# Kernel tuning notes

Measured on AMD Instinct MI355X. Metric: run time of the kernel, lower is better.

Reference implementation:

```python
import jax, jax.numpy as jnp
import numpy as np
import math

B = 8
N_SURF_PER, N_LIG_PER = 5000, 128
N_SURF, N_LIG = B * N_SURF_PER, B * N_LIG_PER
N = N_SURF + N_LIG
HID, TDIM, NLAYERS = 512, 64, 6
E_MAX = 131072
RADIUS = 3.5
BOX = 24.1  # box edge so that radius-3.5 cross-degree ~64


def sinusoidal_emb(t, dim):
    # standard SinusoidalPosEmb: cat(sin, cos) over log-spaced freqs
    half = dim // 2
    freqs = jnp.exp(-math.log(10000.0) / (half - 1) * jnp.arange(half, dtype=t.dtype))
    ang = t[:, None] * freqs[None, :]
    return jnp.concatenate([jnp.sin(ang), jnp.cos(ang)], axis=-1)


def setup_inputs() -> dict:
    rng = np.random.default_rng(0)
    surf = rng.uniform(0.0, BOX, (B, N_SURF_PER, 3)).astype(np.float32)
    lig = rng.uniform(0.0, BOX, (B, N_LIG_PER, 3)).astype(np.float32)
    # radius_graph per batch; only surface->ligand edges survive filter_edges,
    # so we materialize exactly the cross edges (others are filtered to weight 0 anyway)
    srcs, dsts = [], []
    for b in range(B):
        d2 = ((surf[b][:, None, :] - lig[b][None, :, :]) ** 2).sum(-1)
        sj, li = np.nonzero(d2 <= RADIUS ** 2)
        srcs.append(b * N_SURF_PER + sj)
        dsts.append(N_SURF + b * N_LIG_PER + li)
    src = np.concatenate(srcs)
    dst = np.concatenate(dsts)
    E = min(len(src), E_MAX)
    edge_index = np.zeros((2, E_MAX), dtype=np.int32)  # pad with (0,0): filtered out
    edge_index[0, :E] = src[:E]
    edge_index[1, :E] = dst[:E]
    batch_surface = np.repeat(np.arange(B), N_SURF_PER).astype(np.int32)
    batch_ligand = np.repeat(np.arange(B), N_LIG_PER).astype(np.int32)

    ks = jax.random.split(jax.random.key(0), 10)

    def gl(k, shp, fan_in):
        return jax.random.normal(k, shp, jnp.float32) / np.sqrt(fan_in)

    return dict(
        surface_pos=jnp.asarray(surf.reshape(-1, 3)),
        init_ligand_pos=jnp.asarray(lig.reshape(-1, 3)),
        time=jax.random.uniform(ks[9], (N_LIG, 1), jnp.float32) * 1000.0,
        edge_index=jnp.asarray(edge_index),
        batch_surface=jnp.asarray(batch_surface),
        batch_ligand=jnp.asarray(batch_ligand),
        W_surf=gl(ks[0], (3, HID), 3), b_surf=jnp.zeros((HID,), jnp.float32),
        W_t1=gl(ks[1], (TDIM, 4 * TDIM), TDIM), b_t1=jnp.zeros((4 * TDIM,), jnp.float32),
        W_t2=gl(ks[2], (4 * TDIM, TDIM), 4 * TDIM), b_t2=jnp.zeros((TDIM,), jnp.float32),
        W_lig=gl(ks[3], (3, HID), 3), b_lig=jnp.zeros((HID,), jnp.float32),
        W_gate=gl(ks[4], (TDIM, HID), TDIM), b_gate=jnp.zeros((HID,), jnp.float32),
        W_hbias=gl(ks[5], (TDIM, HID), TDIM),
        W_gcn=gl(ks[6], (NLAYERS, HID, HID), HID), b_gcn=jnp.zeros((NLAYERS, HID), jnp.float32),
        W_pos=gl(ks[7], (HID, 3), HID), b_pos=jnp.zeros((3,), jnp.float32),
    )


def reference(surface_pos, init_ligand_pos, time, edge_index, batch_surface, batch_ligand,
              W_surf, b_surf, W_t1, b_t1, W_t2, b_t2, W_lig, b_lig,
              W_gate, b_gate, W_hbias, W_gcn, b_gcn, W_pos, b_pos):
    # encoders
    h_surf = surface_pos @ W_surf + b_surf                      # [N_surf, HID]
    t_emb = sinusoidal_emb(jnp.squeeze(time, -1), TDIM)         # [N_lig, TDIM]
    h_time = jax.nn.gelu(t_emb @ W_t1 + b_t1, approximate=False) @ W_t2 + b_t2
    # ConcatSquashLinear: layer(x)*sigmoid(hyper_gate(ctx)) + hyper_bias(ctx)
    h_lig = ((init_ligand_pos @ W_lig + b_lig)
             * jax.nn.sigmoid(h_time @ W_gate + b_gate)
             + h_time @ W_hbias)                                # [N_lig, HID]

    h_node = jnp.concatenate([h_surf, h_lig], axis=0)           # [N, HID]
    mask_ligand = jnp.concatenate([jnp.zeros((N_SURF,), bool), jnp.ones((N_LIG,), bool)])

    src, dst = edge_index[0], edge_index[1]
    # filter_edges: keep surface -> ligand (padded (0,0) edges killed here too)
    w = ((~mask_ligand[src]) & mask_ligand[dst]).astype(h_node.dtype)  # [E]

    # GCN symmetric norm with self loops (edge weight 1 self loop)
    deg = jnp.ones((N,), h_node.dtype).at[dst].add(w)           # in-degree + 1
    dinv = 1.0 / jnp.sqrt(deg)
    norm = w * dinv[src] * dinv[dst]                            # [E]

    # original loop feeds h_node into every layer; only the last output is kept
    for l in range(NLAYERS):
        xw = h_node @ W_gcn[l]                                  # [N, HID]
        msg = jax.ops.segment_sum(norm[:, None] * xw[src], dst, num_segments=N)
        h_combined = msg + (dinv * dinv)[:, None] * xw + b_gcn[l]

    # mask_ligand selects the trailing ligand block (static slice)
    return h_combined[N_SURF:] @ W_pos + b_pos                  # [N_lig, 3]
```

## Files before the change

### kernel.cpp

```cpp
#include <hip/hip_runtime.h>
#include <math.h>

#define N_SURF 40000
#define N_LIG  1024
#define HID    512
#define TDIM   64
#define E_MAX  131072
#define L5     5

#define WS_WP     0
#define WS_A3     1536
#define WS_BSP    1545
#define WS_BPOUT  1548
#define WS_WHBP   1552
#define WS_AGG    1744
#define WS_CNT    4816
#define WS_ZERO_BEGIN 1744
#define WS_ZERO_COUNT 4096

__global__ void k_prep1(const float* __restrict__ Wgcn, const float* __restrict__ Wpos,
                        float* __restrict__ ws) {
    int lane = threadIdx.x & 63;
    int w    = threadIdx.x >> 6;
    int k    = blockIdx.x * 4 + w;
    const float* Wg5 = Wgcn + (size_t)L5 * HID * HID + (size_t)k * HID;
    float a0 = 0.f, a1 = 0.f, a2 = 0.f;
    for (int j = lane; j < HID; j += 64) {
        float v = Wg5[j];
        a0 += v * Wpos[j * 3 + 0];
        a1 += v * Wpos[j * 3 + 1];
        a2 += v * Wpos[j * 3 + 2];
    }
    for (int m = 32; m; m >>= 1) {
        a0 += __shfl_xor(a0, m);
        a1 += __shfl_xor(a1, m);
        a2 += __shfl_xor(a2, m);
    }
    if (lane == 0) {
        ws[WS_WP + k * 3 + 0] = a0;
        ws[WS_WP + k * 3 + 1] = a1;
        ws[WS_WP + k * 3 + 2] = a2;
    }
    int idx = blockIdx.x * blockDim.x + threadIdx.x;
    if (idx < WS_ZERO_COUNT) ws[WS_ZERO_BEGIN + idx] = 0.f;
}

__global__ __launch_bounds__(256) void k_mid(
    const float* __restrict__ Wsurf, const float* __restrict__ bsurf,
    const float* __restrict__ bgcn,  const float* __restrict__ Wpos,
    const float* __restrict__ bpos,  const float* __restrict__ Whb,
    const int*   __restrict__ ei,    const float* __restrict__ spos,
    float* __restrict__ ws) {
    if (blockIdx.x < 52) {
        int lane = threadIdx.x & 63;
        int w    = threadIdx.x >> 6;
        int o    = blockIdx.x * 4 + w;
        if (o >= 207) return;
        float acc = 0.f;
        if (o < 9) {
            int a = o / 3, jp = o - a * 3;
            for (int k = lane; k < HID; k += 64)
                acc += Wsurf[a * HID + k] * ws[WS_WP + k * 3 + jp];
        } else if (o < 12) {
            int jp = o - 9;
            for (int k = lane; k < HID; k += 64)
                acc += bsurf[k] * ws[WS_WP + k * 3 + jp];
        } else if (o < 15) {
            int jp = o - 12;
            for (int j = lane; j < HID; j += 64)
                acc += bgcn[L5 * HID + j] * Wpos[j * 3 + jp];
        } else {
            int r = (o - 15) / 3, jp = (o - 15) % 3;
            for (int j = lane; j < HID; j += 64)
                acc += Whb[r * HID + j] * ws[WS_WP + j * 3 + jp];
        }
        for (int m = 32; m; m >>= 1) acc += __shfl_xor(acc, m);
        if (lane == 0) {
            if (o < 9)        ws[WS_A3 + o] = acc;
            else if (o < 12)  ws[WS_BSP + (o - 9)] = acc;
            else if (o < 15)  ws[WS_BPOUT + (o - 12)] = acc + bpos[o - 12];
            else              ws[WS_WHBP + (o - 15)] = acc;
        }
    } else {
        int e = (blockIdx.x - 52) * 256 + threadIdx.x;
        int s = ei[e];
        int d = ei[E_MAX + e];
        if (s < N_SURF && d >= N_SURF) {
            int li = d - N_SURF;
            atomicAdd(&ws[WS_AGG + li * 3 + 0], spos[s * 3 + 0]);
            atomicAdd(&ws[WS_AGG + li * 3 + 1], spos[s * 3 + 1]);
            atomicAdd(&ws[WS_AGG + li * 3 + 2], spos[s * 3 + 2]);
            atomicAdd(&ws[WS_CNT + li], 1.0f);
        }
    }
}

__global__ __launch_bounds__(256, 4) void k_lig(
    const float* __restrict__ lpos,  const float* __restrict__ tarr,
    const float* __restrict__ Wt1,   const float* __restrict__ bt1,
    const float* __restrict__ Wt2,   const float* __restrict__ bt2,
    const float* __restrict__ Wlig,  const float* __restrict__ blig,
    const float* __restrict__ Wgate, const float* __restrict__ bgate,
    const float* __restrict__ ws,    float* __restrict__ out)
{
    __shared__ float s_emb[64];
    __shared__ float s_h1[256];
    __shared__ float s_ht[64];
    __shared__ float s_red[256];
    __shared__ float s_out[12];
    int t    = threadIdx.x;
    int lane = t & 63;
    int w    = t >> 6;
    int i    = blockIdx.x;

    float tt = tarr[i];
    if (t < 64) {
        const float coef = -0.29710775f;
        float ang = tt * expf(coef * (float)(t & 31));
        s_emb[t] = (t < 32) ? sinf(ang) : cosf(ang);
    }
    __syncthreads();
    {
        float acc0 = bt1[t], acc1 = 0.f;
        #pragma unroll 16
        for (int k = 0; k < 64; k += 2) {
            acc0 += s_emb[k]     * Wt1[k * 256 + t];
            acc1 += s_emb[k + 1] * Wt1[(k + 1) * 256 + t];
        }
        float acc = acc0 + acc1;
        s_h1[t] = 0.5f * acc * (1.f + erff(acc * 0.70710678f));
    }
    __syncthreads();
    {
        int c0 = w * 64;
        float acc0 = 0.f, acc1 = 0.f;
        #pragma unroll 16
        for (int k = 0; k < 64; k += 2) {
            acc0 += s_h1[c0 + k]     * Wt2[(c0 + k) * 64 + lane];
            acc1 += s_h1[c0 + k + 1] * Wt2[(c0 + k + 1) * 64 + lane];
        }
        s_red[t] = acc0 + acc1;
    }
    __syncthreads();
    if (t < 64) s_ht[t] = bt2[t] + s_red[t] + s_red[t + 64] + s_red[t + 128] + s_red[t + 192];
    __syncthreads();

    float px = lpos[i * 3 + 0], py = lpos[i * 3 + 1], pz = lpos[i * 3 + 2];
    float a0 = 0.f, a1 = 0.f, a2 = 0.f;
    for (int r = 0; r < 2; ++r) {
        int j = r * 256 + t;
        float g0 = bgate[j], g1 = 0.f;
        #pragma unroll 16
        for (int k = 0; k < 64; k += 2) {
            g0 += s_ht[k]     * Wgate[k * 512 + j];
            g1 += s_ht[k + 1] * Wgate[(k + 1) * 512 + j];
        }
        float g  = g0 + g1;
        float p  = blig[j] + px * Wlig[j] + py * Wlig[512 + j] + pz * Wlig[1024 + j];
        float hl = p * (1.f / (1.f + expf(-g)));
        a0 += hl * ws[WS_WP + j * 3 + 0];
        a1 += hl * ws[WS_WP + j * 3 + 1];
        a2 += hl * ws[WS_WP + j * 3 + 2];
    }
    if (t < 64) {
        float ht = s_ht[t];
        a0 += ht * ws[WS_WHBP + t * 3 + 0];
        a1 += ht * ws[WS_WHBP + t * 3 + 1];
        a2 += ht * ws[WS_WHBP + t * 3 + 2];
    }
    for (int m = 32; m; m >>= 1) {
        a0 += __shfl_xor(a0, m);
        a1 += __shfl_xor(a1, m);
        a2 += __shfl_xor(a2, m);
    }
    if (lane == 0) { s_out[w * 3 + 0] = a0; s_out[w * 3 + 1] = a1; s_out[w * 3 + 2] = a2; }
    __syncthreads();
    if (t == 0) {
        float b0 = s_out[0] + s_out[3] + s_out[6] + s_out[9];
        float b1 = s_out[1] + s_out[4] + s_out[7] + s_out[10];
        float b2 = s_out[2] + s_out[5] + s_out[8] + s_out[11];
        float d  = ws[WS_CNT + i];
        float s1 = 1.f / sqrtf(1.f + d);
        float s2 = 1.f / (1.f + d);
        float c  = s1 * d;
        float ax = s1 * ws[WS_AGG + i * 3 + 0];
        float ay = s1 * ws[WS_AGG + i * 3 + 1];
        float az = s1 * ws[WS_AGG + i * 3 + 2];
        float acc[3] = {b0, b1, b2};
        #pragma unroll
        for (int jp = 0; jp < 3; ++jp) {
            out[i * 3 + jp] = ax * ws[WS_A3 + 0 + jp] +
                              ay * ws[WS_A3 + 3 + jp] +
                              az * ws[WS_A3 + 6 + jp] +
                              c  * ws[WS_BSP + jp]    +
                              s2 * acc[jp]            +
                              ws[WS_BPOUT + jp];
        }
    }
}

extern "C" void kernel_launch(void* const* d_in, const int* in_sizes, int n_in,
                              void* d_out, int out_size, void* d_ws, size_t ws_size,
                              hipStream_t stream) {
    const float* spos  = (const float*)d_in[0];
    const float* lpos  = (const float*)d_in[1];
    const float* tarr  = (const float*)d_in[2];
    const int*   ei    = (const int*)  d_in[3];
    const float* Wsurf = (const float*)d_in[6];
    const float* bsurf = (const float*)d_in[7];
    const float* Wt1   = (const float*)d_in[8];
    const float* bt1   = (const float*)d_in[9];
    const float* Wt2   = (const float*)d_in[10];
    const float* bt2   = (const float*)d_in[11];
    const float* Wlig  = (const float*)d_in[12];
    const float* blig  = (const float*)d_in[13];
    const float* Wgate = (const float*)d_in[14];
    const float* bgate = (const float*)d_in[15];
    const float* Whb   = (const float*)d_in[16];
    const float* Wgcn  = (const float*)d_in[17];
    const float* bgcn  = (const float*)d_in[18];
    const float* Wpos  = (const float*)d_in[19];
    const float* bpos  = (const float*)d_in[20];
    float* ws  = (float*)d_ws;
    float* out = (float*)d_out;

    hipLaunchKernelGGL(k_prep1, dim3(128), dim3(256), 0, stream, Wgcn, Wpos, ws);
    hipLaunchKernelGGL(k_mid,   dim3(52 + E_MAX / 256), dim3(256), 0, stream,
                       Wsurf, bsurf, bgcn, Wpos, bpos, Whb, ei, spos, ws);
    hipLaunchKernelGGL(k_lig,   dim3(N_LIG), dim3(256), 0, stream,
                       lpos, tarr, Wt1, bt1, Wt2, bt2, Wlig, blig, Wgate, bgate, ws, out);
}
```

Before: 37.70 us.

## Process four ligands per block in k_lig to reuse weight loads

Each k_lig block now handles four ligand nodes instead of one, so every weight element of Wt1, Wgate, Wlig and the projected Wp is loaded once and applied to four rows held in registers. The second time-MLP layer is restructured so each wavefront computes one ligand's full 256-wide reduction, which removes a shared-memory reduction step and a barrier. The goal is to cut redundant global/L2 weight traffic and launch a quarter as many blocks. In exchange each thread holds more registers and the grid shrinks to 256 blocks, which lowers parallelism on a large GPU.

```diff
diff --git a/kernel.cpp b/kernel.cpp
--- a/kernel.cpp
+++ b/kernel.cpp
@@ -103,82 +103,106 @@
     const float* __restrict__ Wgate, const float* __restrict__ bgate,
     const float* __restrict__ ws,    float* __restrict__ out)
 {
-    __shared__ float s_emb[64];
-    __shared__ float s_h1[256];
-    __shared__ float s_ht[64];
-    __shared__ float s_red[256];
-    __shared__ float s_out[12];
+    __shared__ float s_emb[4][64];
+    __shared__ float s_h1[4][256];
+    __shared__ float s_ht[4][64];
+    __shared__ float s_out[4][4][3];
     int t    = threadIdx.x;
     int lane = t & 63;
     int w    = t >> 6;
-    int i    = blockIdx.x;
-
-    float tt = tarr[i];
-    if (t < 64) {
+    int i0   = blockIdx.x * 4;
+
+    {
+        float tt = tarr[i0 + w];
         const float coef = -0.29710775f;
-        float ang = tt * expf(coef * (float)(t & 31));
-        s_emb[t] = (t < 32) ? sinf(ang) : cosf(ang);
+        float ang = tt * expf(coef * (float)(lane & 31));
+        s_emb[w][lane] = (lane < 32) ? sinf(ang) : cosf(ang);
     }
     __syncthreads();
     {
-        float acc0 = bt1[t], acc1 = 0.f;
+        float b = bt1[t];
+        float acc[4] = {b, b, b, b};
         #pragma unroll 16
-        for (int k = 0; k < 64; k += 2) {
-            acc0 += s_emb[k]     * Wt1[k * 256 + t];
-            acc1 += s_emb[k + 1] * Wt1[(k + 1) * 256 + t];
-        }
-        float acc = acc0 + acc1;
-        s_h1[t] = 0.5f * acc * (1.f + erff(acc * 0.70710678f));
+        for (int k = 0; k < 64; ++k) {
+            float wv = Wt1[k * 256 + t];
+            #pragma unroll
+            for (int n = 0; n < 4; ++n) acc[n] += s_emb[n][k] * wv;
+        }
+        #pragma unroll
+        for (int n = 0; n < 4; ++n)
+            s_h1[n][t] = 0.5f * acc[n] * (1.f + erff(acc[n] * 0.70710678f));
     }
     __syncthreads();
     {
-        int c0 = w * 64;
-        float acc0 = 0.f, acc1 = 0.f;
+        float a0 = 0.f, a1 = 0.f, a2 = 0.f, a3 = 0.f;
         #pragma unroll 16
-        for (int k = 0; k < 64; k += 2) {
-            acc0 += s_h1[c0 + k]     * Wt2[(c0 + k) * 64 + lane];
-            acc1 += s_h1[c0 + k + 1] * Wt2[(c0 + k + 1) * 64 + lane];
-        }
-        s_red[t] = acc0 + acc1;
-    }
-    __syncthreads();
-    if (t < 64) s_ht[t] = bt2[t] + s_red[t] + s_red[t + 64] + s_red[t + 128] + s_red[t + 192];
-    __syncthreads();
-
-    float px = lpos[i * 3 + 0], py = lpos[i * 3 + 1], pz = lpos[i * 3 + 2];
-    float a0 = 0.f, a1 = 0.f, a2 = 0.f;
+        for (int k = 0; k < 256; k += 4) {
+            a0 += s_h1[w][k + 0] * Wt2[(k + 0) * 64 + lane];
+            a1 += s_h1[w][k + 1] * Wt2[(k + 1) * 64 + lane];
+            a2 += s_h1[w][k + 2] * Wt2[(k + 2) * 64 + lane];
+            a3 += s_h1[w][k + 3] * Wt2[(k + 3) * 64 + lane];
+        }
+        s_ht[w][lane] = bt2[lane] + ((a0 + a1) + (a2 + a3));
+    }
+    __syncthreads();
+
+    float px[4], py[4], pz[4];
+    #pragma unroll
+    for (int n = 0; n < 4; ++n) {
+        px[n] = lpos[(i0 + n) * 3 + 0];
+        py[n] = lpos[(i0 + n) * 3 + 1];
+        pz[n] = lpos[(i0 + n) * 3 + 2];
+    }
+    float a[4][3] = {};
+    #pragma unroll
     for (int r = 0; r < 2; ++r) {
         int j = r * 256 + t;
-        float g0 = bgate[j], g1 = 0.f;
+        float bg = bgate[j];
+        float g[4] = {bg, bg, bg, bg};
         #pragma unroll 16
-        for (int k = 0; k < 64; k += 2) {
-            g0 += s_ht[k]     * Wgate[k * 512 + j];
-            g1 += s_ht[k + 1] * Wgate[(k + 1) * 512 + j];
-        }
-        float g  = g0 + g1;
-        float p  = blig[j] + px * Wlig[j] + py * Wlig[512 + j] + pz * Wlig[1024 + j];
-        float hl = p * (1.f / (1.f + expf(-g)));
-        a0 += hl * ws[WS_WP + j * 3 + 0];
-        a1 += hl * ws[WS_WP + j * 3 + 1];
-        a2 += hl * ws[WS_WP + j * 3 + 2];
+        for (int k = 0; k < 64; ++k) {
+            float wv = Wgate[k * 512 + j];
+            #pragma unroll
+            for (int n = 0; n < 4; ++n) g[n] += s_ht[n][k] * wv;
+        }
+        float wl0 = Wlig[j], wl1 = Wlig[512 + j], wl2 = Wlig[1024 + j], bl = blig[j];
+        float wp0 = ws[WS_WP + j * 3 + 0];
+        float wp1 = ws[WS_WP + j * 3 + 1];
+        float wp2 = ws[WS_WP + j * 3 + 2];
+        #pragma unroll
+        for (int n = 0; n < 4; ++n) {
+            float p  = bl + px[n] * wl0 + py[n] * wl1 + pz[n] * wl2;
+            float hl = p * (1.f / (1.f + expf(-g[n])));
+            a[n][0] += hl * wp0;
+            a[n][1] += hl * wp1;
+            a[n][2] += hl * wp2;
+        }
     }
     if (t < 64) {
-        float ht = s_ht[t];
-        a0 += ht * ws[WS_WHBP + t * 3 + 0];
-        a1 += ht * ws[WS_WHBP + t * 3 + 1];
-        a2 += ht * ws[WS_WHBP + t * 3 + 2];
-    }
-    for (int m = 32; m; m >>= 1) {
-        a0 += __shfl_xor(a0, m);
-        a1 += __shfl_xor(a1, m);
-        a2 += __shfl_xor(a2, m);
-    }
-    if (lane == 0) { s_out[w * 3 + 0] = a0; s_out[w * 3 + 1] = a1; s_out[w * 3 + 2] = a2; }
-    __syncthreads();
-    if (t == 0) {
-        float b0 = s_out[0] + s_out[3] + s_out[6] + s_out[9];
-        float b1 = s_out[1] + s_out[4] + s_out[7] + s_out[10];
-        float b2 = s_out[2] + s_out[5] + s_out[8] + s_out[11];
+        float h0 = ws[WS_WHBP + t * 3 + 0];
+        float h1v = ws[WS_WHBP + t * 3 + 1];
+        float h2 = ws[WS_WHBP + t * 3 + 2];
+        #pragma unroll
+        for (int n = 0; n < 4; ++n) {
+            float ht = s_ht[n][t];
+            a[n][0] += ht * h0;
+            a[n][1] += ht * h1v;
+            a[n][2] += ht * h2;
+        }
+    }
+    #pragma unroll
+    for (int n = 0; n < 4; ++n)
+        #pragma unroll
+        for (int jp = 0; jp < 3; ++jp)
+            for (int m = 32; m; m >>= 1) a[n][jp] += __shfl_xor(a[n][jp], m);
+    if (lane == 0)
+        #pragma unroll
+        for (int n = 0; n < 4; ++n)
+            #pragma unroll
+            for (int jp = 0; jp < 3; ++jp) s_out[w][n][jp] = a[n][jp];
+    __syncthreads();
+    if (t < 4) {
+        int n = t, i = i0 + n;
         float d  = ws[WS_CNT + i];
         float s1 = 1.f / sqrtf(1.f + d);
         float s2 = 1.f / (1.f + d);
@@ -186,14 +210,14 @@
         float ax = s1 * ws[WS_AGG + i * 3 + 0];
         float ay = s1 * ws[WS_AGG + i * 3 + 1];
         float az = s1 * ws[WS_AGG + i * 3 + 2];
-        float acc[3] = {b0, b1, b2};
         #pragma unroll
         for (int jp = 0; jp < 3; ++jp) {
+            float b = s_out[0][n][jp] + s_out[1][n][jp] + s_out[2][n][jp] + s_out[3][n][jp];
             out[i * 3 + jp] = ax * ws[WS_A3 + 0 + jp] +
                               ay * ws[WS_A3 + 3 + jp] +
                               az * ws[WS_A3 + 6 + jp] +
                               c  * ws[WS_BSP + jp]    +
-                              s2 * acc[jp]            +
+                              s2 * b                  +
                               ws[WS_BPOUT + jp];
         }
     }
@@ -227,6 +251,6 @@
     hipLaunchKernelGGL(k_prep1, dim3(128), dim3(256), 0, stream, Wgcn, Wpos, ws);
     hipLaunchKernelGGL(k_mid,   dim3(52 + E_MAX / 256), dim3(256), 0, stream,
                        Wsurf, bsurf, bgcn, Wpos, bpos, Whb, ei, spos, ws);
-    hipLaunchKernelGGL(k_lig,   dim3(N_LIG), dim3(256), 0, stream,
+    hipLaunchKernelGGL(k_lig,   dim3(N_LIG / 4), dim3(256), 0, stream,
                        lpos, tarr, Wt1, bt1, Wt2, bt2, Wlig, blig, Wgate, bgate, ws, out);
 }
```

Measured after the change: 38.24 us. No clear change (+1.4%).
